# Kernel optimization log

Measured on AMD Instinct MI355X. Metric: run time of the kernel, lower is better.

## Reference

```python
import jax, jax.numpy as jnp
import numpy as np

B, N, H, D = 16, 128, 32, 5            # graphs, entities, heads, multi_hop_max_dist
NUM_EDGES, NUM_SPATIAL, NUM_EDGE_DIS = 1536, 512, 128
HID, NEF = 768, 3                       # hidden dim (unused in math), edge feats


def setup_inputs() -> dict:
    key = jax.random.key(0)
    ks = jax.random.split(key, 8)
    x = jax.random.normal(ks[0], (B, N, HID), jnp.float32)
    attn_bias = jax.random.normal(ks[1], (B, N + 1, N + 1), jnp.float32)
    spatial_pos = jax.random.randint(ks[2], (B, N, N), 0, NUM_SPATIAL)
    edge_input = jax.random.randint(ks[3], (B, N, N, D, NEF), 0, NUM_EDGES + 1)
    # embedding tables (std=0.02 init; padding_idx=0 rows zeroed)
    edge_encoder_w = (0.02 * jax.random.normal(ks[4], (NUM_EDGES + 1, H), jnp.float32)).at[0].set(0.0)
    structural_w = (0.02 * jax.random.normal(ks[5], (NUM_SPATIAL, H), jnp.float32)).at[0].set(0.0)
    edge_dis_w = 0.02 * jax.random.normal(ks[6], (NUM_EDGE_DIS * H * H, 1), jnp.float32)
    virt_w = 0.02 * jax.random.normal(ks[7], (1, H), jnp.float32)
    return {"x": x, "attn_bias": attn_bias, "spatial_pos": spatial_pos,
            "edge_input": edge_input, "edge_encoder_w": edge_encoder_w,
            "structural_w": structural_w, "edge_dis_w": edge_dis_w, "virt_w": virt_w}


def reference(x, attn_bias, spatial_pos, edge_input, edge_encoder_w, structural_w, edge_dis_w, virt_w):
    n_graph, n_entity = x.shape[:2]
    # [B, H, N+1, N+1]
    bias = jnp.broadcast_to(attn_bias[:, None], (n_graph, H, n_entity + 1, n_entity + 1))
    # structural (spatial) encoding on the NxN sub-block
    sp_bias = structural_w[spatial_pos].transpose(0, 3, 1, 2)          # [B,H,N,N]
    bias = bias.at[:, :, 1:, 1:].add(sp_bias)
    # graph-token virtual distance
    t = virt_w.reshape(1, H, 1)
    bias = bias.at[:, :, 1:, 0].add(t)
    bias = bias.at[:, :, 0, :].add(t)
    # ---- multi_hop relational encoding ----
    sp = jnp.where(spatial_pos == 0, 1, spatial_pos)
    sp = jnp.where(sp > 1, sp - 1, sp)
    sp = jnp.clip(sp, 0, D)                                            # [B,N,N]
    ei = edge_input[:, :, :, :D, :]                                    # [B,N,N,D,F]
    ei = edge_encoder_w[ei].mean(-2)                                   # [B,N,N,D,H]
    # per-hop head-mixing: bmm over hop dim
    Wdis = edge_dis_w.reshape(-1, H, H)[:D]                            # [D,H,H]
    ei = jnp.einsum('bijdh,dhk->bijdk', ei, Wdis)                      # [B,N,N,D,H]
    ei = ei.sum(-2) / sp[..., None].astype(ei.dtype)                   # [B,N,N,H]
    ei = ei.transpose(0, 3, 1, 2)                                      # [B,H,N,N]
    bias = bias.at[:, :, 1:, 1:].add(ei)
    # final residual add of raw attn_bias
    bias = bias + attn_bias[:, None]
    return bias
```

## Files before the change

### kernel.cpp

```cpp
#include <hip/hip_runtime.h>
#include <hip/hip_bf16.h>

#define B_   16
#define N_   128
#define H_   32
#define D_   5
#define NEF_ 3
#define NE1  1537
#define NP1  129

__global__ __launch_bounds__(256) void fused_tab_kernel(
    const float* __restrict__ edge_encoder_w,
    const float* __restrict__ edge_dis_w,
    __hip_bfloat16* __restrict__ fused)
{
    __shared__ float wd[32 * 32];
    const int tid = threadIdx.x;
    const int bx  = blockIdx.x;
    const int d     = bx / 193;
    const int chunk = bx % 193;

    const float* wsrc = edge_dis_w + d * 1024;
    for (int k = tid; k < 1024; k += 256) wd[k] = wsrc[k];
    __syncthreads();

    const int g    = tid >> 5;
    const int lane = tid & 31;
    const int idx  = chunk * 8 + g;
    if (idx >= NE1) return;

    float w = edge_encoder_w[idx * 32 + lane];
    float acc = 0.f;
    #pragma unroll
    for (int hh = 0; hh < 32; ++hh) {
        acc += __shfl(w, hh, 32) * wd[hh * 32 + lane];
    }
    fused[(d * NE1 + idx) * 32 + lane] = __float2bfloat16(acc);
}

__global__ __launch_bounds__(256) void main_kernel(
    const float* __restrict__ attn_bias,
    const int*   __restrict__ spatial_pos,
    const int*   __restrict__ edge_input,
    const float* __restrict__ structural_w,
    const __hip_bfloat16* __restrict__ fused,
    float* __restrict__ out)
{
    __shared__ float tile[32][33];

    const int bx   = blockIdx.x;
    const int jt   = bx & 3;
    const int i    = (bx >> 2) & 127;
    const int b    = bx >> 9;
    const int tid  = threadIdx.x;
    const int wv   = __builtin_amdgcn_readfirstlane(tid >> 6);
    const int lane = tid & 63;
    const int h    = lane & 31;
    const int hi   = (lane >> 5) & 1;
    const int mhi  = -hi;
    const int h2   = h * 2;
    const int h4   = h * 4;

    const int cell0 = (b * N_ + i) * N_ + jt * 32 + wv * 8;

    #pragma unroll
    for (int pj = 0; pj < 4; ++pj) {
        const int cellA = cell0 + 2 * pj;
        const int* eip  = edge_input + cellA * (D_ * NEF_);
        const int spA = spatial_pos[cellA];
        const int spB = spatial_pos[cellA + 1];

        float acc = 0.f;
        #pragma unroll
        for (int t = 0; t < 15; ++t) {
            const int dbase = (t / 3) * NE1;
            const int offA  = (dbase + eip[t])      << 6;
            const int offB  = (dbase + eip[15 + t]) << 6;
            const int delta = offB - offA;
            const int off   = (delta & mhi) + offA + h2;
            const unsigned short u =
                *(const unsigned short*)((const char*)fused + off);
            union { unsigned int ui; float f; } cv;
            cv.ui = ((unsigned int)u) << 16;
            acc += cv.f;
        }

        int sA = (spA == 0) ? 1 : spA; if (sA > 1) sA -= 1; if (sA > D_) sA = D_;
        int sB = (spB == 0) ? 1 : spB; if (sB > 1) sB -= 1; if (sB > D_) sB = D_;
        const float invA = __builtin_amdgcn_rcpf(3.0f * (float)sA);
        const float invB = __builtin_amdgcn_rcpf(3.0f * (float)sB);
        const float inv  = hi ? invB : invA;

        const int spoff = ((((spB - spA) & mhi) + spA) << 7) + h4;
        const float st = *(const float*)((const char*)structural_w + spoff);

        tile[h][wv * 8 + 2 * pj + hi] = acc * inv + st;
    }
    __syncthreads();

    const int g2 = tid >> 5;
    const int l2 = tid & 31;
    const int j  = jt * 32 + l2 + 1;
    const float ab2 = 2.0f * attn_bias[(b * NP1 + (i + 1)) * NP1 + j];
    #pragma unroll
    for (int rr = 0; rr < 4; ++rr) {
        const int hh = g2 + rr * 8;
        out[((b * H_ + hh) * NP1 + (i + 1)) * NP1 + j] = ab2 + tile[hh][l2];
    }
}

__global__ __launch_bounds__(256) void border_kernel(
    const float* __restrict__ attn_bias,
    const float* __restrict__ virt_w,
    float* __restrict__ out)
{
    const int bh = blockIdx.x;
    const int b = bh >> 5;
    const int h = bh & 31;
    const float t = virt_w[h];

    float*       ob = out + (b * H_ + h) * NP1 * NP1;
    const float* ab = attn_bias + b * NP1 * NP1;

    for (int idx = threadIdx.x; idx < NP1 + N_; idx += 256) {
        if (idx < NP1) {
            ob[idx] = 2.0f * ab[idx] + t;
        } else {
            const int i = idx - 128;
            ob[i * NP1] = 2.0f * ab[i * NP1] + t;
        }
    }
}

extern "C" void kernel_launch(void* const* d_in, const int* in_sizes, int n_in,
                              void* d_out, int out_size, void* d_ws, size_t ws_size,
                              hipStream_t stream) {
    const float* attn_bias      = (const float*)d_in[1];
    const int*   spatial_pos    = (const int*)  d_in[2];
    const int*   edge_input     = (const int*)  d_in[3];
    const float* edge_encoder_w = (const float*)d_in[4];
    const float* structural_w   = (const float*)d_in[5];
    const float* edge_dis_w     = (const float*)d_in[6];
    const float* virt_w         = (const float*)d_in[7];
    float* out = (float*)d_out;
    __hip_bfloat16* fused = (__hip_bfloat16*)d_ws;

    hipLaunchKernelGGL(fused_tab_kernel, dim3(5 * 193), dim3(256), 0, stream,
                       edge_encoder_w, edge_dis_w, fused);
    hipLaunchKernelGGL(main_kernel, dim3(B_ * N_ * 4), dim3(256), 0, stream,
                       attn_bias, spatial_pos, edge_input, structural_w, fused, out);
    hipLaunchKernelGGL(border_kernel, dim3(B_ * H_), dim3(256), 0, stream,
                       attn_bias, virt_w, out);
}
```

Before: 118.0 us.

## Vectorize fused-table gathers with cooperative index loading and lane-shuffle reduction

```diff
diff --git a/kernel.cpp b/kernel.cpp
--- a/kernel.cpp
+++ b/kernel.cpp
@@ -8,6 +8,10 @@
 #define NEF_ 3
 #define NE1  1537
 #define NP1  129
+
+static __device__ __forceinline__ float bits2f(unsigned int u) {
+    union { unsigned int ui; float f; } cv; cv.ui = u; return cv.f;
+}
 
 __global__ __launch_bounds__(256) void fused_tab_kernel(
     const float* __restrict__ edge_encoder_w,
@@ -46,7 +50,7 @@
     const __hip_bfloat16* __restrict__ fused,
     float* __restrict__ out)
 {
-    __shared__ float tile[32][33];
+    __shared__ float tile2[32][36];
 
     const int bx   = blockIdx.x;
     const int jt   = bx & 3;
@@ -55,46 +59,71 @@
     const int tid  = threadIdx.x;
     const int wv   = __builtin_amdgcn_readfirstlane(tid >> 6);
     const int lane = tid & 63;
-    const int h    = lane & 31;
-    const int hi   = (lane >> 5) & 1;
+    const int hi   = lane >> 5;
     const int mhi  = -hi;
-    const int h2   = h * 2;
-    const int h4   = h * 4;
+
+    const int t    = lane & 15;
+    const int c    = (lane >> 4) & 1;
+    const bool vld = (lane < 32) && (t < 15);
+    const int pre  = c * 15 + t;
+    const int d_   = (t >= 3) + (t >= 6) + (t >= 9) + (t >= 12);
+    const int dbase = d_ * (NE1 * 64);
+    const int grp  = (lane >> 3) & 3;
+    const int bp0  = ((hi << 4) + grp) << 2;
+    const int hsub = (lane & 7) * 8;
+    const int h0b  = (lane & 7) * 16;
+    const bool wr  = ((lane & 24) == 0);
 
     const int cell0 = (b * N_ + i) * N_ + jt * 32 + wv * 8;
 
     #pragma unroll
-    for (int pj = 0; pj < 4; ++pj) {
-        const int cellA = cell0 + 2 * pj;
+    for (int p = 0; p < 4; ++p) {
+        const int cellA = cell0 + 2 * p;
         const int* eip  = edge_input + cellA * (D_ * NEF_);
+
+        int idx = 0;
+        if (vld) idx = eip[pre];
+        const int rowoff = (idx << 6) + dbase;
+
+        float a0 = 0.f, a1 = 0.f, a2 = 0.f, a3 = 0.f;
+        #pragma unroll
+        for (int k = 0; k < 4; ++k) {
+            const int ro = __builtin_amdgcn_ds_bpermute(bp0 + 16 * k, rowoff);
+            const unsigned long long w =
+                *(const unsigned long long*)((const char*)fused + (ro + hsub));
+            const unsigned int d0 = (unsigned int)w;
+            const unsigned int d1 = (unsigned int)(w >> 32);
+            a0 += bits2f(d0 << 16);
+            a1 += bits2f(d0 & 0xFFFF0000u);
+            a2 += bits2f(d1 << 16);
+            a3 += bits2f(d1 & 0xFFFF0000u);
+        }
+
+        a0 += __shfl_xor(a0, 8);  a1 += __shfl_xor(a1, 8);
+        a2 += __shfl_xor(a2, 8);  a3 += __shfl_xor(a3, 8);
+        a0 += __shfl_xor(a0, 16); a1 += __shfl_xor(a1, 16);
+        a2 += __shfl_xor(a2, 16); a3 += __shfl_xor(a3, 16);
+
         const int spA = spatial_pos[cellA];
         const int spB = spatial_pos[cellA + 1];
-
-        float acc = 0.f;
-        #pragma unroll
-        for (int t = 0; t < 15; ++t) {
-            const int dbase = (t / 3) * NE1;
-            const int offA  = (dbase + eip[t])      << 6;
-            const int offB  = (dbase + eip[15 + t]) << 6;
-            const int delta = offB - offA;
-            const int off   = (delta & mhi) + offA + h2;
-            const unsigned short u =
-                *(const unsigned short*)((const char*)fused + off);
-            union { unsigned int ui; float f; } cv;
-            cv.ui = ((unsigned int)u) << 16;
-            acc += cv.f;
-        }
-
         int sA = (spA == 0) ? 1 : spA; if (sA > 1) sA -= 1; if (sA > D_) sA = D_;
         int sB = (spB == 0) ? 1 : spB; if (sB > 1) sB -= 1; if (sB > D_) sB = D_;
         const float invA = __builtin_amdgcn_rcpf(3.0f * (float)sA);
         const float invB = __builtin_amdgcn_rcpf(3.0f * (float)sB);
         const float inv  = hi ? invB : invA;
 
-        const int spoff = ((((spB - spA) & mhi) + spA) << 7) + h4;
-        const float st = *(const float*)((const char*)structural_w + spoff);
+        const int spoff = ((((spB - spA) & mhi) + spA) << 7) + h0b;
+        const float4 st = *(const float4*)((const char*)structural_w + spoff);
 
-        tile[h][wv * 8 + 2 * pj + hi] = acc * inv + st;
+        if (wr) {
+            const int jl = wv * 8 + 2 * p + hi;
+            float4 res;
+            res.x = a0 * inv + st.x;
+            res.y = a1 * inv + st.y;
+            res.z = a2 * inv + st.z;
+            res.w = a3 * inv + st.w;
+            *(float4*)&tile2[jl][(lane & 7) * 4] = res;
+        }
     }
     __syncthreads();
 
@@ -105,7 +134,7 @@
     #pragma unroll
     for (int rr = 0; rr < 4; ++rr) {
         const int hh = g2 + rr * 8;
-        out[((b * H_ + hh) * NP1 + (i + 1)) * NP1 + j] = ab2 + tile[hh][l2];
+        out[((b * H_ + hh) * NP1 + (i + 1)) * NP1 + j] = ab2 + tile2[l2][hh];
     }
 }
 
```

Measured after the change: 119.8 us. Within noise of the previous version (+1.6%).
